# Kernel optimization log

Measured on AMD Instinct MI355X. Metric: run time of the kernel, lower is better.

Reference implementation:

```python
import jax, jax.numpy as jnp
import numpy as np

N = 50000   # nodes
E = 500000  # edges
G = 64      # graphs in batch
H = 2       # attention heads
D = 64      # hidden per head (hid)
F_IN = 4    # num_features
C = 5       # num_classes
NEG_SLOPE = 0.2


def setup_inputs() -> dict:
    key = jax.random.key(0)
    ks = jax.random.split(key, 24)
    inp = {
        'x': jax.random.normal(ks[0], (N, F_IN), jnp.float32),
        'edge_index': jax.random.randint(ks[1], (2, E), 0, N, dtype=jnp.int64),
        'batch': jnp.sort(jax.random.randint(ks[2], (N,), 0, G, dtype=jnp.int64)),
    }
    ins = [F_IN, H * D, H * D, H * D]
    ki = 3
    for l, fin in enumerate(ins, 1):
        s = 1.0 / np.sqrt(fin)
        inp[f'W{l}'] = s * jax.random.normal(ks[ki], (fin, H * D), jnp.float32); ki += 1
        inp[f'asrc{l}'] = 0.1 * jax.random.normal(ks[ki], (H, D), jnp.float32); ki += 1
        inp[f'adst{l}'] = 0.1 * jax.random.normal(ks[ki], (H, D), jnp.float32); ki += 1
        inp[f'b{l}'] = 0.01 * jax.random.normal(ks[ki], (H * D,), jnp.float32); ki += 1
    inp['lin_w'] = (1.0 / np.sqrt(H * D)) * jax.random.normal(ks[ki], (H * D, C), jnp.float32); ki += 1
    inp['lin_b'] = jnp.zeros((C,), jnp.float32)
    return inp


def gat_conv(x, src, dst, W, a_src, a_dst, b):
    # x: [N, Fin] -> h: [N, H, D]
    h = (x @ W).reshape(-1, H, D)
    alpha_src = jnp.sum(h * a_src, axis=-1)  # [N, H]
    alpha_dst = jnp.sum(h * a_dst, axis=-1)  # [N, H]
    e = jax.nn.leaky_relu(alpha_src[src] + alpha_dst[dst], NEG_SLOPE)  # [E, H]
    # segment softmax over incoming edges of each dst node
    e_max = jax.ops.segment_max(e, dst, num_segments=N)  # [N, H]
    e_exp = jnp.exp(e - e_max[dst])
    denom = jax.ops.segment_sum(e_exp, dst, num_segments=N)
    alpha = e_exp / (denom[dst] + 1e-16)  # [E, H]
    msg = h[src] * alpha[:, :, None]  # [E, H, D]
    out = jax.ops.segment_sum(msg, dst, num_segments=N)  # [N, H, D]
    return out.reshape(-1, H * D) + b


def reference(x, edge_index, batch,
              W1, asrc1, adst1, b1,
              W2, asrc2, adst2, b2,
              W3, asrc3, adst3, b3,
              W4, asrc4, adst4, b4,
              lin_w, lin_b):
    src, dst = edge_index[0], edge_index[1]
    h = jax.nn.relu(gat_conv(x, src, dst, W1, asrc1, adst1, b1))
    h = jax.nn.relu(gat_conv(h, src, dst, W2, asrc2, adst2, b2))
    h = jax.nn.relu(gat_conv(h, src, dst, W3, asrc3, adst3, b3))
    h = jax.nn.relu(gat_conv(h, src, dst, W4, asrc4, adst4, b4))
    # global mean pool over graphs
    sums = jax.ops.segment_sum(h, batch, num_segments=G)  # [G, 128]
    counts = jax.ops.segment_sum(jnp.ones((h.shape[0],), h.dtype), batch, num_segments=G)
    pooled = sums / jnp.maximum(counts, 1.0)[:, None]
    return jax.nn.sigmoid(pooled @ lin_w + lin_b)  # [G, C]
```

## Files before the change

kernel.cpp:

```cpp
#include <hip/hip_runtime.h>
#include <math.h>

#define NHEAD 2
#define NDIM  64
#define HD    128
#define NGRAPH 64
#define NCLS  5
#define NEG_SLOPE 0.2f
#define LDA 136

typedef __attribute__((ext_vector_type(8))) short bf16x8;
typedef __attribute__((ext_vector_type(4))) float f32x4;

static __device__ __forceinline__ unsigned short f2bf(float f) {
    unsigned int u = __float_as_uint(f);
    u = (u + 0x7fff + ((u >> 16) & 1)) >> 16;
    return (unsigned short)u;
}
static __device__ __forceinline__ float bf2f(unsigned short b) {
    return __uint_as_float((unsigned int)b << 16);
}


__global__ void k_deg(const int* __restrict__ dst, int* __restrict__ deg, int E) {
    int i = blockIdx.x * blockDim.x + threadIdx.x;
    if (i < E) atomicAdd(&deg[dst[i]], 1);
}

__global__ __launch_bounds__(256) void k_scan_local(const int* __restrict__ deg,
                                                    int* __restrict__ ptr,
                                                    int* __restrict__ bsum, int n) {
    __shared__ int wsum[4];
    const int tid = threadIdx.x, lane = tid & 63, wid = tid >> 6;
    const int base = blockIdx.x * 2048 + tid * 8;
    int v[8];
    #pragma unroll
    for (int k = 0; k < 8; ++k) {
        int i = base + k;
        v[k] = (i < n) ? deg[i] : 0;
    }
    #pragma unroll
    for (int k = 1; k < 8; ++k) v[k] += v[k - 1];
    int x = v[7];
    #pragma unroll
    for (int off = 1; off < 64; off <<= 1) {
        int t = __shfl_up(x, off, 64);
        if (lane >= off) x += t;
    }
    if (lane == 63) wsum[wid] = x;
    __syncthreads();
    int woff = 0;
    #pragma unroll
    for (int k = 0; k < 4; ++k) woff += (k < wid) ? wsum[k] : 0;
    int texcl = woff + x - v[7];
    #pragma unroll
    for (int k = 0; k < 8; ++k) {
        int i = base + k;
        if (i < n) ptr[i + 1] = texcl + v[k];
    }
    if (tid == 255) bsum[blockIdx.x] = woff + x;
    if (blockIdx.x == 0 && tid == 0) ptr[0] = 0;
}

__global__ void k_scan_bsum(int* __restrict__ bsum, int B) {
    int lane = threadIdx.x;
    int carry = 0;
    for (int base = 0; base < B; base += 64) {
        int i = base + lane;
        int v = (i < B) ? bsum[i] : 0;
        int x = v;
        #pragma unroll
        for (int off = 1; off < 64; off <<= 1) {
            int t = __shfl_up(x, off, 64);
            if (lane >= off) x += t;
        }
        if (i < B) bsum[i] = carry + x - v;
        carry += __shfl(x, 63, 64);
    }
}

__global__ __launch_bounds__(256) void k_scan_add(int* __restrict__ ptr,
                                                  const int* __restrict__ bsum, int n) {
    int off = bsum[blockIdx.x];
    if (off == 0) return;
    const int base = blockIdx.x * 2048 + threadIdx.x * 8;
    #pragma unroll
    for (int k = 0; k < 8; ++k) {
        int i = base + k;
        if (i < n) ptr[i + 1] += off;
    }
}

__global__ void k_scatter(const int* __restrict__ src, const int* __restrict__ dst,
                          const int* __restrict__ ptr, int* __restrict__ fill,
                          int* __restrict__ csr, int E) {
    int i = blockIdx.x * blockDim.x + threadIdx.x;
    if (i < E) {
        int d = dst[i];
        int pos = atomicAdd(&fill[d], 1);
        csr[ptr[d] + pos] = src[i];
    }
}


__global__ void k_prepw(const float* __restrict__ W2, const float* __restrict__ W3,
                        const float* __restrict__ W4, unsigned short* __restrict__ Wt) {
    int idx = blockIdx.x * blockDim.x + threadIdx.x;
    if (idx >= 3 * HD * HD) return;
    int l = idx / (HD * HD), rem = idx % (HD * HD);
    int n = rem >> 7, k = rem & 127;
    const float* W = (l == 0) ? W2 : (l == 1) ? W3 : W4;
    Wt[idx] = f2bf(W[k * HD + n]);
}

__global__ void k_gemm1_alpha(const float* __restrict__ x, const float* __restrict__ W,
                              const float* __restrict__ asrc, const float* __restrict__ adst,
                              unsigned short* __restrict__ out, float* __restrict__ oas,
                              float* __restrict__ oad, int N) {
    int n = (blockIdx.x * blockDim.x + threadIdx.x) >> 6;
    int lane = threadIdx.x & 63;
    if (n >= N) return;
    float4 xv = *(const float4*)&x[n * 4];
    int c0 = lane * 2;
    float2 w0 = *(const float2*)&W[c0];
    float2 w1 = *(const float2*)&W[128 + c0];
    float2 w2 = *(const float2*)&W[256 + c0];
    float2 w3 = *(const float2*)&W[384 + c0];
    float v0 = xv.x * w0.x + xv.y * w1.x + xv.z * w2.x + xv.w * w3.x;
    float v1 = xv.x * w0.y + xv.y * w1.y + xv.z * w2.y + xv.w * w3.y;
    unsigned short b0 = f2bf(v0), b1 = f2bf(v1);
    unsigned int packed = (unsigned int)b0 | ((unsigned int)b1 << 16);
    *(unsigned int*)&out[(size_t)n * HD + c0] = packed;
    float vx = bf2f(b0), vy = bf2f(b1);
    float2 av = *(const float2*)&asrc[c0];
    float2 dv = *(const float2*)&adst[c0];
    float s = vx * av.x + vy * av.y;
    float t = vx * dv.x + vy * dv.y;
    #pragma unroll
    for (int off = 16; off > 0; off >>= 1) {
        s += __shfl_xor(s, off);
        t += __shfl_xor(t, off);
    }
    if ((lane & 31) == 0) {
        int head = lane >> 5;
        oas[n * 2 + head] = s;
        oad[n * 2 + head] = t;
    }
}

static __device__ __forceinline__ uint4 agg_row(
    const unsigned short* __restrict__ h, const float* __restrict__ oas,
    const float* __restrict__ oad, const int* __restrict__ ptr,
    const int* __restrict__ csr, const float* __restrict__ bias,
    int n, int N, int sub, int gbase, int hsel) {
    const bool valid = (n < N);
    int beg = 0, end = 0;
    float2 adn = make_float2(0.f, 0.f);
    if (valid) {
        beg = ptr[n]; end = ptr[n + 1];
        adn = *(const float2*)&oad[n * 2];
    }
    float m0 = -INFINITY, m1 = -INFINITY, l0 = 0.f, l1 = 0.f;
    float acc[8];
    #pragma unroll
    for (int k = 0; k < 8; ++k) acc[k] = 0.f;

    auto accum = [&](uint4 hv, float pj) {
        #pragma unroll
        for (int k = 0; k < 4; ++k) {
            unsigned int u = (&hv.x)[k];
            acc[2 * k]     += pj * __uint_as_float(u << 16);
            acc[2 * k + 1] += pj * __uint_as_float(u & 0xffff0000u);
        }
    };

    int cbeg = beg;
    while (__any(cbeg < end)) {
        int rem = end - cbeg;
        int cnt = rem < 0 ? 0 : (rem > 16 ? 16 : rem);
        int s = 0;
        float e0 = -INFINITY, e1 = -INFINITY;
        if (sub < cnt) {
            s = csr[cbeg + sub];
            float2 as = *(const float2*)&oas[s * 2];
            e0 = as.x + adn.x; e0 = (e0 >= 0.f) ? e0 : NEG_SLOPE * e0;
            e1 = as.y + adn.y; e1 = (e1 >= 0.f) ? e1 : NEG_SLOPE * e1;
        }
        float c0 = e0, c1 = e1;
        #pragma unroll
        for (int off = 8; off > 0; off >>= 1) {
            c0 = fmaxf(c0, __shfl_xor(c0, off));
            c1 = fmaxf(c1, __shfl_xor(c1, off));
        }
        float nm0 = fmaxf(m0, c0), nm1 = fmaxf(m1, c1);
        float sc0 = (nm0 == -INFINITY) ? 0.f : __expf(m0 - nm0);
        float sc1 = (nm1 == -INFINITY) ? 0.f : __expf(m1 - nm1);
        float p0 = (sub < cnt) ? __expf(e0 - nm0) : 0.f;
        float p1 = (sub < cnt) ? __expf(e1 - nm1) : 0.f;
        float s0 = p0, s1 = p1;
        #pragma unroll
        for (int off = 8; off > 0; off >>= 1) {
            s0 += __shfl_xor(s0, off);
            s1 += __shfl_xor(s1, off);
        }
        l0 = l0 * sc0 + s0;
        l1 = l1 * sc1 + s1;
        m0 = nm0; m1 = nm1;
        float scl = hsel ? sc1 : sc0;
        #pragma unroll
        for (int k = 0; k < 8; ++k) acc[k] *= scl;

        int jm = cnt;
        jm = max(jm, __shfl_xor(jm, 16));
        jm = max(jm, __shfl_xor(jm, 32));

        auto fetchp = [&](int j, uint4& hv, float& pj) {
            int sj = __shfl(s, gbase + j);
            float pa = __shfl(p0, gbase + j);
            float pb = __shfl(p1, gbase + j);
            pj = hsel ? pb : pa;
            hv = make_uint4(0, 0, 0, 0);
            if (j < cnt)
                hv = *(const uint4*)&h[(size_t)sj * HD + sub * 8];
        };
        uint4 hA, hB = make_uint4(0, 0, 0, 0);
        float pA, pB = 0.f;
        fetchp(0, hA, pA);
        if (jm > 1) fetchp(1, hB, pB);
        for (int j = 2; j < jm; ++j) {
            uint4 hC; float pC;
            fetchp(j, hC, pC);
            accum(hA, pA);
            hA = hB; pA = pB;
            hB = hC; pB = pC;
        }
        accum(hA, pA);
        if (jm > 1) accum(hB, pB);

        cbeg += 16;
    }

    uint4 pk = make_uint4(0, 0, 0, 0);
    if (valid) {
        float lsel = hsel ? l1 : l0;
        float inv = 1.f / (lsel + 1e-16f);
        float4 ba = *(const float4*)&bias[sub * 8];
        float4 bb = *(const float4*)&bias[sub * 8 + 4];
        float o[8];
        o[0] = fmaxf(acc[0] * inv + ba.x, 0.f);
        o[1] = fmaxf(acc[1] * inv + ba.y, 0.f);
        o[2] = fmaxf(acc[2] * inv + ba.z, 0.f);
        o[3] = fmaxf(acc[3] * inv + ba.w, 0.f);
        o[4] = fmaxf(acc[4] * inv + bb.x, 0.f);
        o[5] = fmaxf(acc[5] * inv + bb.y, 0.f);
        o[6] = fmaxf(acc[6] * inv + bb.z, 0.f);
        o[7] = fmaxf(acc[7] * inv + bb.w, 0.f);
        pk.x = (unsigned int)f2bf(o[0]) | ((unsigned int)f2bf(o[1]) << 16);
        pk.y = (unsigned int)f2bf(o[2]) | ((unsigned int)f2bf(o[3]) << 16);
        pk.z = (unsigned int)f2bf(o[4]) | ((unsigned int)f2bf(o[5]) << 16);
        pk.w = (unsigned int)f2bf(o[6]) | ((unsigned int)f2bf(o[7]) << 16);
    }
    return pk;
}

__global__ __launch_bounds__(256) void k_agg_gemm(
    const unsigned short* __restrict__ hin,
    const float* __restrict__ oas_in, const float* __restrict__ oad_in,
    const int* __restrict__ ptr, const int* __restrict__ csr,
    const float* __restrict__ bias,
    const unsigned short* __restrict__ Wt,
    const float* __restrict__ asrc, const float* __restrict__ adst,
    unsigned short* __restrict__ hout,
    float* __restrict__ oas_out, float* __restrict__ oad_out, int N) {
    __shared__ unsigned short As[64 * LDA];
    const int tid = threadIdx.x;
    const int lane = tid & 63, w = tid >> 6;
    const int grp = lane >> 4, sub = lane & 15;
    const int gbase = lane & 48;
    const int hsel = sub >> 3;
    const int nbase = blockIdx.x * 64;

    #pragma unroll 1
    for (int p = 0; p < 4; ++p) {
        const int row = w * 16 + p * 4 + grp;
        uint4 pk = agg_row(hin, oas_in, oad_in, ptr, csr, bias,
                           nbase + row, N, sub, gbase, hsel);
        *(uint4*)&As[(size_t)row * LDA + sub * 8] = pk;
    }
    __syncthreads();

    float av[8], dv[8];
    #pragma unroll
    for (int c = 0; c < 8; ++c) {
        av[c] = asrc[c * 16 + sub];
        dv[c] = adst[c * 16 + sub];
    }
    f32x4 acc[8];
    #pragma unroll
    for (int c = 0; c < 8; ++c) acc[c] = (f32x4)(0.f);

    #pragma unroll
    for (int ks = 0; ks < 4; ++ks) {
        bf16x8 a0 = *(const bf16x8*)&As[(size_t)(w * 16 + sub) * LDA + ks * 32 + grp * 8];
        #pragma unroll
        for (int c = 0; c < 8; ++c) {
            bf16x8 b = *(const bf16x8*)&Wt[(size_t)(c * 16 + sub) * HD + ks * 32 + grp * 8];
            acc[c] = __builtin_amdgcn_mfma_f32_16x16x32_bf16(a0, b, acc[c], 0, 0, 0);
        }
    }

    const int rowb = nbase + w * 16 + grp * 4;
    #pragma unroll
    for (int c = 0; c < 8; ++c) {
        f32x4 v = acc[c];
        int col = c * 16 + sub;
        #pragma unroll
        for (int r = 0; r < 4; ++r) {
            int row = rowb + r;
            if (row < N) hout[(size_t)row * HD + col] = f2bf(v[r]);
        }
    }
    #pragma unroll
    for (int r = 0; r < 4; ++r) {
        float ps0 = 0.f, ps1 = 0.f, pd0 = 0.f, pd1 = 0.f;
        #pragma unroll
        for (int c = 0; c < 4; ++c) {
            float hv = acc[c][r];
            ps0 += hv * av[c]; pd0 += hv * dv[c];
        }
        #pragma unroll
        for (int c = 4; c < 8; ++c) {
            float hv = acc[c][r];
            ps1 += hv * av[c]; pd1 += hv * dv[c];
        }
        #pragma unroll
        for (int off = 1; off < 16; off <<= 1) {
            ps0 += __shfl_xor(ps0, off);
            ps1 += __shfl_xor(ps1, off);
            pd0 += __shfl_xor(pd0, off);
            pd1 += __shfl_xor(pd1, off);
        }
        int row = rowb + r;
        if (sub == 0 && row < N) {
            *(float2*)&oas_out[row * 2] = make_float2(ps0, ps1);
            *(float2*)&oad_out[row * 2] = make_float2(pd0, pd1);
        }
    }
}

__global__ __launch_bounds__(256) void k_agg_final(
    const unsigned short* __restrict__ hin,
    const float* __restrict__ oas_in, const float* __restrict__ oad_in,
    const int* __restrict__ ptr, const int* __restrict__ csr,
    const float* __restrict__ bias,
    unsigned short* __restrict__ out, int N) {
    const int tid = threadIdx.x;
    const int lane = tid & 63;
    const int grp = lane >> 4, sub = lane & 15;
    const int gbase = lane & 48;
    const int hsel = sub >> 3;
    const int n = ((blockIdx.x * blockDim.x + tid) >> 6) * 4 + grp;
    uint4 pk = agg_row(hin, oas_in, oad_in, ptr, csr, bias, n, N, sub, gbase, hsel);
    if (n < N) *(uint4*)&out[(size_t)n * HD + sub * 8] = pk;
}

__global__ void k_pool(const unsigned short* __restrict__ feat, const int* __restrict__ batch,
                       float* __restrict__ pooled, int* __restrict__ gcount, int N) {
    int col = threadIdx.x;
    int n0 = blockIdx.x * 128;
    int n1 = min(n0 + 128, N);
    float acc = 0.f;
    int curg = -1, runlen = 0;
    for (int n = n0; n < n1; ++n) {
        int g = batch[n];
        if (g != curg) {
            if (curg >= 0) {
                atomicAdd(&pooled[curg * HD + col], acc);
                if (col == 0) atomicAdd(&gcount[curg], runlen);
            }
            acc = 0.f; runlen = 0;
            curg = g;
        }
        acc += bf2f(feat[(size_t)n * HD + col]);
        runlen++;
    }
    if (curg >= 0) {
        atomicAdd(&pooled[curg * HD + col], acc);
        if (col == 0) atomicAdd(&gcount[curg], runlen);
    }
}

__global__ void k_final(const float* __restrict__ pooled, const int* __restrict__ gcount,
                        const float* __restrict__ lw, const float* __restrict__ lb,
                        float* __restrict__ out) {
    int tid = threadIdx.x;
    if (tid >= NGRAPH * NCLS) return;
    int g = tid / NCLS, c = tid % NCLS;
    float cnt = fmaxf((float)gcount[g], 1.f);
    const float* p = pooled + g * HD;
    float sum = 0.f;
    for (int k = 0; k < HD; ++k)
        sum += p[k] * lw[k * NCLS + c];
    float z = lb[c] + sum / cnt;
    out[tid] = 1.f / (1.f + __expf(-z));
}


static inline size_t al256(size_t x) { return (x + 255) & ~(size_t)255; }

extern "C" void kernel_launch(void* const* d_in, const int* in_sizes, int n_in,
                              void* d_out, int out_size, void* d_ws, size_t ws_size,
                              hipStream_t stream) {
    const int N = in_sizes[0] / 4;
    const int E = in_sizes[1] / 2;

    const float* x     = (const float*)d_in[0];
    const int*   esrc  = (const int*)d_in[1];
    const int*   edst  = esrc + E;
    const int*   batch = (const int*)d_in[2];
    const float* Wl[4]  = {(const float*)d_in[3],  (const float*)d_in[7],
                           (const float*)d_in[11], (const float*)d_in[15]};
    const float* asr[4] = {(const float*)d_in[4],  (const float*)d_in[8],
                           (const float*)d_in[12], (const float*)d_in[16]};
    const float* ads[4] = {(const float*)d_in[5],  (const float*)d_in[9],
                           (const float*)d_in[13], (const float*)d_in[17]};
    const float* bs[4]  = {(const float*)d_in[6],  (const float*)d_in[10],
                           (const float*)d_in[14], (const float*)d_in[18]};
    const float* lin_w = (const float*)d_in[19];
    const float* lin_b = (const float*)d_in[20];
    float* out = (float*)d_out;

    char* w = (char*)d_ws;
    size_t off = 0;
    auto alloc = [&](size_t bytes) -> void* {
        void* p = w + off;
        off = al256(off + bytes);
        return p;
    };
    int*   deg    = (int*)alloc((size_t)N * 4);
    int*   fill   = (int*)alloc((size_t)N * 4);
    int*   gcount = (int*)alloc((size_t)NGRAPH * 4);
    float* pooled = (float*)alloc((size_t)NGRAPH * HD * 4);
    size_t zbytes = off;
    int*   ptr    = (int*)alloc((size_t)(N + 1) * 4);
    int*   bsum   = (int*)alloc((size_t)1024 * 4);
    int*   csr    = (int*)alloc((size_t)E * 4);
    unsigned short* hA   = (unsigned short*)alloc((size_t)N * HD * 2);
    unsigned short* hB   = (unsigned short*)alloc((size_t)N * HD * 2);
    unsigned short* feat = (unsigned short*)alloc((size_t)N * HD * 2);
    unsigned short* Wt   = (unsigned short*)alloc((size_t)3 * HD * HD * 2);
    float* asA = (float*)alloc((size_t)N * 2 * 4);
    float* adA = (float*)alloc((size_t)N * 2 * 4);
    float* asB = (float*)alloc((size_t)N * 2 * 4);
    float* adB = (float*)alloc((size_t)N * 2 * 4);
    (void)ws_size; (void)n_in; (void)out_size;

    hipMemsetAsync(d_ws, 0, zbytes, stream);

    k_prepw<<<(3 * HD * HD + 255) / 256, 256, 0, stream>>>(Wl[1], Wl[2], Wl[3], Wt);
    k_deg<<<(E + 255) / 256, 256, 0, stream>>>(edst, deg, E);
    const int SB = (N + 2047) / 2048;
    k_scan_local<<<SB, 256, 0, stream>>>(deg, ptr, bsum, N);
    k_scan_bsum<<<1, 64, 0, stream>>>(bsum, SB);
    k_scan_add<<<SB, 256, 0, stream>>>(ptr, bsum, N);
    k_scatter<<<(E + 255) / 256, 256, 0, stream>>>(esrc, edst, ptr, fill, csr, E);

    const int fused_blocks = (N + 63) / 64;

    k_gemm1_alpha<<<(N + 3) / 4, 256, 0, stream>>>(
        x, Wl[0], asr[0], ads[0], hA, asA, adA, N);
    k_agg_gemm<<<fused_blocks, 256, 0, stream>>>(
        hA, asA, adA, ptr, csr, bs[0], Wt,
        asr[1], ads[1], hB, asB, adB, N);
    k_agg_gemm<<<fused_blocks, 256, 0, stream>>>(
        hB, asB, adB, ptr, csr, bs[1], Wt + (size_t)HD * HD,
        asr[2], ads[2], hA, asA, adA, N);
    k_agg_gemm<<<fused_blocks, 256, 0, stream>>>(
        hA, asA, adA, ptr, csr, bs[2], Wt + (size_t)2 * HD * HD,
        asr[3], ads[3], hB, asB, adB, N);
    k_agg_final<<<(N + 15) / 16, 256, 0, stream>>>(
        hB, asB, adB, ptr, csr, bs[3], feat, N);

    k_pool<<<(N + 127) / 128, 128, 0, stream>>>(feat, batch, pooled, gcount, N);
    k_final<<<1, 320, 0, stream>>>(pooled, gcount, lin_w, lin_b, out);
}
```

Before: 390.5 us.

## Shrink fused agg-gemm tile to 16 rows and split output columns across waves

```diff
diff --git a/kernel.cpp b/kernel.cpp
--- a/kernel.cpp
+++ b/kernel.cpp
@@ -263,7 +263,7 @@
     return pk;
 }
 
-__global__ __launch_bounds__(256) void k_agg_gemm(
+__global__ __launch_bounds__(256, 8) void k_agg_gemm(
     const unsigned short* __restrict__ hin,
     const float* __restrict__ oas_in, const float* __restrict__ oad_in,
     const int* __restrict__ ptr, const int* __restrict__ csr,
@@ -272,78 +272,75 @@
     const float* __restrict__ asrc, const float* __restrict__ adst,
     unsigned short* __restrict__ hout,
     float* __restrict__ oas_out, float* __restrict__ oad_out, int N) {
-    __shared__ unsigned short As[64 * LDA];
+    __shared__ unsigned short As[16 * LDA];
+    __shared__ float psL[4][16], pdL[4][16];
     const int tid = threadIdx.x;
     const int lane = tid & 63, w = tid >> 6;
     const int grp = lane >> 4, sub = lane & 15;
     const int gbase = lane & 48;
     const int hsel = sub >> 3;
-    const int nbase = blockIdx.x * 64;
-
-    #pragma unroll 1
-    for (int p = 0; p < 4; ++p) {
-        const int row = w * 16 + p * 4 + grp;
-        uint4 pk = agg_row(hin, oas_in, oad_in, ptr, csr, bias,
-                           nbase + row, N, sub, gbase, hsel);
-        *(uint4*)&As[(size_t)row * LDA + sub * 8] = pk;
-    }
+    const int nbase = blockIdx.x * 16;
+
+    const int row = w * 4 + grp;
+    uint4 pk = agg_row(hin, oas_in, oad_in, ptr, csr, bias,
+                       nbase + row, N, sub, gbase, hsel);
+    *(uint4*)&As[(size_t)row * LDA + sub * 8] = pk;
     __syncthreads();
 
-    float av[8], dv[8];
-    #pragma unroll
-    for (int c = 0; c < 8; ++c) {
-        av[c] = asrc[c * 16 + sub];
-        dv[c] = adst[c * 16 + sub];
-    }
-    f32x4 acc[8];
-    #pragma unroll
-    for (int c = 0; c < 8; ++c) acc[c] = (f32x4)(0.f);
-
+    float av2[2], dv2[2];
+    #pragma unroll
+    for (int i = 0; i < 2; ++i) {
+        int c = w * 2 + i;
+        av2[i] = asrc[c * 16 + sub];
+        dv2[i] = adst[c * 16 + sub];
+    }
+    f32x4 acc[2];
+    acc[0] = (f32x4)(0.f);
+    acc[1] = (f32x4)(0.f);
     #pragma unroll
     for (int ks = 0; ks < 4; ++ks) {
-        bf16x8 a0 = *(const bf16x8*)&As[(size_t)(w * 16 + sub) * LDA + ks * 32 + grp * 8];
-        #pragma unroll
-        for (int c = 0; c < 8; ++c) {
+        bf16x8 a0 = *(const bf16x8*)&As[(size_t)sub * LDA + ks * 32 + grp * 8];
+        #pragma unroll
+        for (int i = 0; i < 2; ++i) {
+            int c = w * 2 + i;
             bf16x8 b = *(const bf16x8*)&Wt[(size_t)(c * 16 + sub) * HD + ks * 32 + grp * 8];
-            acc[c] = __builtin_amdgcn_mfma_f32_16x16x32_bf16(a0, b, acc[c], 0, 0, 0);
-        }
-    }
-
-    const int rowb = nbase + w * 16 + grp * 4;
-    #pragma unroll
-    for (int c = 0; c < 8; ++c) {
-        f32x4 v = acc[c];
-        int col = c * 16 + sub;
+            acc[i] = __builtin_amdgcn_mfma_f32_16x16x32_bf16(a0, b, acc[i], 0, 0, 0);
+        }
+    }
+
+    const int rowb = nbase + grp * 4;
+    #pragma unroll
+    for (int i = 0; i < 2; ++i) {
+        int col = (w * 2 + i) * 16 + sub;
         #pragma unroll
         for (int r = 0; r < 4; ++r) {
-            int row = rowb + r;
-            if (row < N) hout[(size_t)row * HD + col] = f2bf(v[r]);
+            int rw = rowb + r;
+            if (rw < N) hout[(size_t)rw * HD + col] = f2bf(acc[i][r]);
         }
     }
     #pragma unroll
     for (int r = 0; r < 4; ++r) {
-        float ps0 = 0.f, ps1 = 0.f, pd0 = 0.f, pd1 = 0.f;
-        #pragma unroll
-        for (int c = 0; c < 4; ++c) {
-            float hv = acc[c][r];
-            ps0 += hv * av[c]; pd0 += hv * dv[c];
-        }
-        #pragma unroll
-        for (int c = 4; c < 8; ++c) {
-            float hv = acc[c][r];
-            ps1 += hv * av[c]; pd1 += hv * dv[c];
-        }
+        float ps = acc[0][r] * av2[0] + acc[1][r] * av2[1];
+        float pd = acc[0][r] * dv2[0] + acc[1][r] * dv2[1];
         #pragma unroll
         for (int off = 1; off < 16; off <<= 1) {
-            ps0 += __shfl_xor(ps0, off);
-            ps1 += __shfl_xor(ps1, off);
-            pd0 += __shfl_xor(pd0, off);
-            pd1 += __shfl_xor(pd1, off);
-        }
-        int row = rowb + r;
-        if (sub == 0 && row < N) {
-            *(float2*)&oas_out[row * 2] = make_float2(ps0, ps1);
-            *(float2*)&oad_out[row * 2] = make_float2(pd0, pd1);
+            ps += __shfl_xor(ps, off);
+            pd += __shfl_xor(pd, off);
+        }
+        if (sub == 0) {
+            psL[w][grp * 4 + r] = ps;
+            pdL[w][grp * 4 + r] = pd;
+        }
+    }
+    __syncthreads();
+    if (tid < 32) {
+        int r2 = tid & 15, head = tid >> 4;
+        int n2 = nbase + r2;
+        if (n2 < N) {
+            float s = psL[2 * head][r2] + psL[2 * head + 1][r2];
+            float d = pdL[2 * head][r2] + pdL[2 * head + 1][r2];
+            oas_out[n2 * 2 + head] = s;
+            oad_out[n2 * 2 + head] = d;
         }
     }
 }
@@ -465,7 +462,7 @@
     k_scan_add<<<SB, 256, 0, stream>>>(ptr, bsum, N);
     k_scatter<<<(E + 255) / 256, 256, 0, stream>>>(esrc, edst, ptr, fill, csr, E);
 
-    const int fused_blocks = (N + 63) / 64;
+    const int fused_blocks = (N + 15) / 16;
 
     k_gemm1_alpha<<<(N + 3) / 4, 256, 0, stream>>>(
         x, Wl[0], asr[0], ads[0], hA, asA, adA, N);
```

Result: faster. 371.4 us (-4.9%).
